# Kernel optimization log

Measured on AMD Instinct MI355X. Metric: run time of the kernel, lower is better.

The kernel has to match this reference:

```python
import jax, jax.numpy as jnp
import numpy as np

B, T, C = 2, 2048, 2048
H, HKV, D = 16, 4, 128
THETA = 10000.0
G = H // HKV  # kv groups


def _rope_tables(seq_len, dim, theta):
    inv_freq = 1.0 / theta ** (jnp.arange(0, dim, 2, dtype=jnp.float32) / dim)
    t = jnp.arange(seq_len, dtype=jnp.float32)
    freqs = jnp.outer(t, inv_freq)                 # [T, D/2]
    emb = jnp.concatenate([freqs, freqs], axis=-1)  # [T, D]
    return jnp.cos(emb)[None, None], jnp.sin(emb)[None, None]  # [1,1,T,D]


def _rotate_half(x):
    x1, x2 = jnp.split(x, 2, axis=-1)
    return jnp.concatenate([-x2, x1], axis=-1)


def setup_inputs() -> dict:
    key = jax.random.key(0)
    ks = jax.random.split(key, 6)
    x = jax.random.normal(ks[0], (B, T, C), dtype=jnp.float32)
    s = 0.02
    Wq = jax.random.normal(ks[1], (C, H * D), dtype=jnp.float32) * s
    Wk = jax.random.normal(ks[2], (C, HKV * D), dtype=jnp.float32) * s
    Wv = jax.random.normal(ks[3], (C, HKV * D), dtype=jnp.float32) * s
    Wo = jax.random.normal(ks[4], (H * D, C), dtype=jnp.float32) * s
    mask = jnp.tril(jnp.ones((T, T), dtype=jnp.int32))[None, None]  # causal [1,1,T,T]
    return {"x": x, "Wq": Wq, "Wk": Wk, "Wv": Wv, "Wo": Wo, "mask": mask}


def reference(x, Wq, Wk, Wv, Wo, mask):
    b, t, _ = x.shape
    q = (x @ Wq).reshape(b, t, H, D).transpose(0, 2, 1, 3)      # [B,H,T,D]
    k = (x @ Wk).reshape(b, t, HKV, D).transpose(0, 2, 1, 3)    # [B,HKV,T,D]
    v = (x @ Wv).reshape(b, t, HKV, D).transpose(0, 2, 1, 3)
    cos, sin = _rope_tables(t, D, THETA)
    q = q * cos + _rotate_half(q) * sin
    k = k * cos + _rotate_half(k) * sin
    # expand kv heads (repeat_interleave over head axis)
    k = jnp.repeat(k, G, axis=1)                                # [B,H,T,D]
    v = jnp.repeat(v, G, axis=1)
    attn = jnp.einsum('bhqd,bhkd->bhqk', q, k) / jnp.sqrt(jnp.float32(D))
    attn = jnp.where(mask == 0, jnp.float32(-jnp.inf), attn)
    attn = jax.nn.softmax(attn, axis=-1)
    out = jnp.einsum('bhqk,bhkd->bhqd', attn, v)                # [B,H,T,D]
    out = out.transpose(0, 2, 1, 3).reshape(b, t, H * D)
    return out @ Wo
```

## Files before the change

### kernel.cpp

```cpp
#include <hip/hip_runtime.h>
#include <math.h>

#define B_ 2
#define T_ 2048
#define C_ 2048
#define H_ 16
#define HKV_ 4
#define D_ 128
#define G_ (H_ / HKV_)
#define GK 2048

typedef float f32x4 __attribute__((ext_vector_type(4)));
typedef __bf16 bf16x8 __attribute__((ext_vector_type(8)));

static __device__ __forceinline__ f32x4 mfma16(bf16x8 a, bf16x8 b, f32x4 c) {
    return __builtin_amdgcn_mfma_f32_16x16x32_bf16(a, b, c, 0, 0, 0);
}

__global__ __launch_bounds__(256)
void conv_f32_bf16(const float* __restrict__ src, __bf16* __restrict__ dst, int n8)
{
    const int i = blockIdx.x * blockDim.x + threadIdx.x;
    if (i >= n8) return;
    const float4 a = *(const float4*)&src[(size_t)i * 8];
    const float4 b = *(const float4*)&src[(size_t)i * 8 + 4];
    bf16x8 o;
    o[0] = (__bf16)a.x; o[1] = (__bf16)a.y; o[2] = (__bf16)a.z; o[3] = (__bf16)a.w;
    o[4] = (__bf16)b.x; o[5] = (__bf16)b.y; o[6] = (__bf16)b.z; o[7] = (__bf16)b.w;
    *(bf16x8*)&dst[(size_t)i * 8] = o;
}

__global__ __launch_bounds__(256)
void tconv(const float* __restrict__ src, __bf16* __restrict__ dst, int N)
{
    __shared__ __bf16 tl[32][34];
    const int tx = threadIdx.x;
    const int ty = threadIdx.y;
    const int k0 = blockIdx.x * 32;
    const int n0 = blockIdx.y * 32;

    #pragma unroll
    for (int i = 0; i < 4; ++i) {
        const int r = ty + i * 8;
        tl[r][tx] = (__bf16)src[(size_t)(k0 + r) * N + n0 + tx];
    }
    __syncthreads();
    #pragma unroll
    for (int i = 0; i < 4; ++i) {
        const int r = ty + i * 8;
        dst[(size_t)(n0 + r) * GK + k0 + tx] = tl[tx][r];
    }
}

#define LSTR 72

#define GEMM_MAIN(At, Bt)                                                       \
    __shared__ __bf16 As[128 * LSTR];                                           \
    __shared__ __bf16 Bs[128 * LSTR];                                           \
    const int tid = threadIdx.x;                                                \
    const int wave = tid >> 6, lane = tid & 63;                                 \
    const int a = lane & 15, bq = lane >> 4;                                    \
    const int wr = wave >> 1, wc = wave & 1;                                    \
    f32x4 acc[4][4];                                                            \
    _Pragma("unroll")                                                           \
    for (int mi = 0; mi < 4; ++mi)                                              \
        _Pragma("unroll")                                                       \
        for (int ni = 0; ni < 4; ++ni) acc[mi][ni] = (f32x4){0.f,0.f,0.f,0.f};  \
    for (int k0 = 0; k0 < GK; k0 += 64) {                                       \
        __syncthreads();                                                        \
        _Pragma("unroll")                                                       \
        for (int i = 0; i < 4; ++i) {                                           \
            const int idx = i * 256 + tid;                                      \
            const int r = idx >> 3, c8 = (idx & 7) * 8;                         \
            *(bf16x8*)&As[r * LSTR + c8] =                                      \
                *(const bf16x8*)&(At)[(size_t)r * GK + k0 + c8];                \
            *(bf16x8*)&Bs[r * LSTR + c8] =                                      \
                *(const bf16x8*)&(Bt)[(size_t)r * GK + k0 + c8];                \
        }                                                                       \
        __syncthreads();                                                        \
        _Pragma("unroll")                                                       \
        for (int ks = 0; ks < 2; ++ks) {                                        \
            bf16x8 af[4], bfr[4];                                               \
            _Pragma("unroll")                                                   \
            for (int mi = 0; mi < 4; ++mi)                                      \
                af[mi] = *(const bf16x8*)&As[(wr*64 + mi*16 + a) * LSTR + ks*32 + bq*8]; \
            _Pragma("unroll")                                                   \
            for (int ni = 0; ni < 4; ++ni)                                      \
                bfr[ni] = *(const bf16x8*)&Bs[(wc*64 + ni*16 + a) * LSTR + ks*32 + bq*8]; \
            _Pragma("unroll")                                                   \
            for (int mi = 0; mi < 4; ++mi)                                      \
                _Pragma("unroll")                                               \
                for (int ni = 0; ni < 4; ++ni)                                  \
                    acc[mi][ni] = mfma16(af[mi], bfr[ni], acc[mi][ni]);         \
        }                                                                       \
    }

__global__ __launch_bounds__(256)
void gemm_qkv_mfma(const __bf16* __restrict__ xb,
                   const __bf16* __restrict__ wqt,
                   const __bf16* __restrict__ wkt,
                   const __bf16* __restrict__ wvt,
                   __bf16* __restrict__ qbuf,
                   __bf16* __restrict__ kbuf,
                   __bf16* __restrict__ vbuf)
{
    const int n0 = blockIdx.x * 128;
    const int m0 = blockIdx.y * 128;
    const __bf16* Btp; __bf16* outb; int NH, nloc;
    if (n0 < 2048)      { Btp = wqt + (size_t)n0 * GK;          outb = qbuf; NH = 16; nloc = n0; }
    else if (n0 < 2560) { Btp = wkt + (size_t)(n0 - 2048) * GK; outb = kbuf; NH = 4;  nloc = n0 - 2048; }
    else                { Btp = wvt + (size_t)(n0 - 2560) * GK; outb = vbuf; NH = 4;  nloc = n0 - 2560; }
    const __bf16* Atp = xb + (size_t)m0 * GK;

    GEMM_MAIN(Atp, Btp)

    const int b  = m0 >> 11;
    const int t0 = m0 & (T_ - 1);
    const int h0 = nloc >> 7;
    __bf16* op = outb + (size_t)(b * NH + h0) * T_ * D_;
    #pragma unroll
    for (int mi = 0; mi < 4; ++mi)
        #pragma unroll
        for (int ni = 0; ni < 4; ++ni)
            #pragma unroll
            for (int rr = 0; rr < 4; ++rr) {
                const int row = t0 + wr * 64 + mi * 16 + bq * 4 + rr;
                const int col = wc * 64 + ni * 16 + a;
                op[(size_t)row * D_ + col] = (__bf16)acc[mi][ni][rr];
            }
}

__global__ __launch_bounds__(256)
void gemm_out_mfma(const __bf16* __restrict__ ab,
                   const __bf16* __restrict__ wot,
                   float* __restrict__ outp)
{
    const int n0 = blockIdx.x * 128;
    const int m0 = blockIdx.y * 128;
    const __bf16* Atp = ab + (size_t)m0 * GK;
    const __bf16* Btp = wot + (size_t)n0 * GK;

    GEMM_MAIN(Atp, Btp)

    #pragma unroll
    for (int mi = 0; mi < 4; ++mi)
        #pragma unroll
        for (int ni = 0; ni < 4; ++ni)
            #pragma unroll
            for (int rr = 0; rr < 4; ++rr) {
                const int row = m0 + wr * 64 + mi * 16 + bq * 4 + rr;
                const int col = n0 + wc * 64 + ni * 16 + a;
                outp[(size_t)row * C_ + col] = acc[mi][ni][rr];
            }
}

__global__ void rope_bf16(__bf16* __restrict__ buf)
{
    const int idx = blockIdx.x * blockDim.x + threadIdx.x;
    const int jj  = idx & 31;
    const int row = idx >> 5;
    const int t   = row & (T_ - 1);
    const int d   = jj * 2;

    const float LOG_THETA = 9.210340371976184f;
    const float f1 = (float)t * __expf(-(float)d       * (LOG_THETA / 64.0f));
    const float f2 = (float)t * __expf(-(float)(d + 1) * (LOG_THETA / 64.0f));
    float s1, c1, s2, c2;
    __sincosf(f1, &s1, &c1);
    __sincosf(f2, &s2, &c2);

    __bf16* p = buf + (size_t)row * D_ + d;
    const float x1a = (float)p[0],  x1b = (float)p[1];
    const float x2a = (float)p[64], x2b = (float)p[65];
    p[0]  = (__bf16)(x1a * c1 - x2a * s1);
    p[1]  = (__bf16)(x1b * c2 - x2b * s2);
    p[64] = (__bf16)(x2a * c1 + x1a * s1);
    p[65] = (__bf16)(x2b * c2 + x1b * s2);
}

__global__ __launch_bounds__(256)
void transpose_v(const __bf16* __restrict__ vb, __bf16* __restrict__ vtb)
{
    __shared__ __bf16 tl[32][33];
    const int tx = threadIdx.x;
    const int ty = threadIdx.y;
    const int t0 = blockIdx.x * 32;
    const int d0 = blockIdx.y * 32;
    const int bh = blockIdx.z;

    const __bf16* src = vb + ((size_t)bh * T_ + t0) * D_ + d0;
    #pragma unroll
    for (int i = 0; i < 4; ++i) {
        const int r = ty + i * 8;
        tl[r][tx] = src[(size_t)r * D_ + tx];
    }
    __syncthreads();
    __bf16* dst = vtb + ((size_t)bh * D_ + d0) * T_ + t0;
    #pragma unroll
    for (int i = 0; i < 4; ++i) {
        const int dl = ty + i * 8;
        dst[(size_t)dl * T_ + tx] = tl[tx][dl];
    }
}

#define KS_STRIDE 136
#define PS_STRIDE 76

__global__ __launch_bounds__(512)
void flash_attn_mfma(const __bf16* __restrict__ qb,
                     const __bf16* __restrict__ kb,
                     const __bf16* __restrict__ vtb,
                     __bf16* __restrict__ abuf)
{
    __shared__ __bf16 KsL[64 * KS_STRIDE];
    __shared__ __bf16 VsL[2 * 128 * 4 * 8];
    __shared__ __bf16 PsL[8 * 16 * PS_STRIDE];

    const int tid  = threadIdx.x;
    const int wave = tid >> 6;
    const int lane = tid & 63;
    const int a    = lane & 15;
    const int bq   = lane >> 4;

    const int pair = blockIdx.x;
    const int bh   = blockIdx.y;
    const int b    = bh >> 4;
    const int h    = bh & 15;
    const int kvh  = h >> 2;

    const __bf16* kg  = kb  + (size_t)(b * HKV_ + kvh) * T_ * D_;
    const __bf16* vtg = vtb + (size_t)(b * HKV_ + kvh) * D_ * T_;

    const float scale = 0.08838834764831845f;

    for (int half = 0; half < 2; ++half) {
        const int qti = half == 0 ? (15 - pair) : pair;
        const int qt0 = qti * 128;
        const int ntiles = 2 * qti + 2;

        const __bf16* qg = qb + ((size_t)(b * H_ + h) * T_ + qt0 + wave * 16) * D_;
        bf16x8 qf[4];
        #pragma unroll
        for (int ks = 0; ks < 4; ++ks)
            qf[ks] = *(const bf16x8*)&qg[(size_t)a * D_ + ks * 32 + bq * 8];

        f32x4 oacc[8];
        #pragma unroll
        for (int dt = 0; dt < 8; ++dt) oacc[dt] = (f32x4){0.f, 0.f, 0.f, 0.f};
        float m_r[4] = {-INFINITY, -INFINITY, -INFINITY, -INFINITY};
        float l_r[4] = {0.f, 0.f, 0.f, 0.f};

        bf16x8 kpre[2], vpre[2];
        #pragma unroll
        for (int it = 0; it < 2; ++it) {
            const int idx = it * 512 + tid;
            const int r = idx >> 4, c8 = (idx & 15) * 8;
            kpre[it] = *(const bf16x8*)&kg[(size_t)r * D_ + c8];
            const int bo = idx & 3, dd = (idx >> 2) & 127, ss2 = idx >> 9;
            vpre[it] = *(const bf16x8*)&vtg[(size_t)dd * T_ + ss2 * 32 + bo * 8];
        }
        __syncthreads();
        #pragma unroll
        for (int it = 0; it < 2; ++it) {
            const int idx = it * 512 + tid;
            const int r = idx >> 4, c8 = (idx & 15) * 8;
            *(bf16x8*)&KsL[r * KS_STRIDE + c8] = kpre[it];
            *(bf16x8*)&VsL[idx * 8] = vpre[it];
        }
        __syncthreads();

        for (int kt = 0; kt < ntiles; ++kt) {
            const int k0 = kt * 64;
            if (kt + 1 < ntiles) {
                const int k0n = k0 + 64;
                #pragma unroll
                for (int it = 0; it < 2; ++it) {
                    const int idx = it * 512 + tid;
                    const int r = idx >> 4, c8 = (idx & 15) * 8;
                    kpre[it] = *(const bf16x8*)&kg[(size_t)(k0n + r) * D_ + c8];
                    const int bo = idx & 3, dd = (idx >> 2) & 127, ss2 = idx >> 9;
                    vpre[it] = *(const bf16x8*)&vtg[(size_t)dd * T_ + k0n + ss2 * 32 + bo * 8];
                }
            }

            f32x4 sacc[4];
            #pragma unroll
            for (int nt = 0; nt < 4; ++nt) {
                sacc[nt] = (f32x4){0.f, 0.f, 0.f, 0.f};
                #pragma unroll
                for (int ks = 0; ks < 4; ++ks) {
                    bf16x8 kf = *(const bf16x8*)&KsL[(nt * 16 + a) * KS_STRIDE + ks * 32 + bq * 8];
                    sacc[nt] = mfma16(qf[ks], kf, sacc[nt]);
                }
            }

            float p[4][4];
            float mrow[4] = {-INFINITY, -INFINITY, -INFINITY, -INFINITY};
            #pragma unroll
            for (int nt = 0; nt < 4; ++nt) {
                const int kc = k0 + nt * 16 + a;
                #pragma unroll
                for (int r = 0; r < 4; ++r) {
                    const int qrow = qt0 + wave * 16 + bq * 4 + r;
                    float s = sacc[nt][r] * scale;
                    s = (kc <= qrow) ? s : -INFINITY;
                    p[nt][r] = s;
                    mrow[r] = fmaxf(mrow[r], s);
                }
            }
            #pragma unroll
            for (int off = 1; off < 16; off <<= 1)
                #pragma unroll
                for (int r = 0; r < 4; ++r)
                    mrow[r] = fmaxf(mrow[r], __shfl_xor(mrow[r], off));

            float corr[4], psum[4];
            #pragma unroll
            for (int r = 0; r < 4; ++r) {
                const float mnew = fmaxf(m_r[r], mrow[r]);
                corr[r] = __expf(m_r[r] - mnew);
                m_r[r] = mnew;
                psum[r] = 0.f;
                #pragma unroll
                for (int nt = 0; nt < 4; ++nt) {
                    const float pe = __expf(p[nt][r] - mnew);
                    p[nt][r] = pe;
                    psum[r] += pe;
                }
            }
            #pragma unroll
            for (int off = 1; off < 16; off <<= 1)
                #pragma unroll
                for (int r = 0; r < 4; ++r)
                    psum[r] += __shfl_xor(psum[r], off);
            #pragma unroll
            for (int r = 0; r < 4; ++r) l_r[r] = l_r[r] * corr[r] + psum[r];

            #pragma unroll
            for (int dt = 0; dt < 8; ++dt)
                #pragma unroll
                for (int r = 0; r < 4; ++r) oacc[dt][r] *= corr[r];

            #pragma unroll
            for (int nt = 0; nt < 4; ++nt)
                #pragma unroll
                for (int r = 0; r < 4; ++r)
                    PsL[(wave * 16 + bq * 4 + r) * PS_STRIDE + nt * 16 + a] = (__bf16)p[nt][r];

            bf16x8 pf[2];
            #pragma unroll
            for (int ss = 0; ss < 2; ++ss)
                pf[ss] = *(const bf16x8*)&PsL[(wave * 16 + a) * PS_STRIDE + ss * 32 + bq * 8];
            #pragma unroll
            for (int dt = 0; dt < 8; ++dt) {
                #pragma unroll
                for (int ss = 0; ss < 2; ++ss) {
                    bf16x8 vf = *(const bf16x8*)&VsL[ss * 4096 + (dt * 16 + a) * 32 + bq * 8];
                    oacc[dt] = mfma16(pf[ss], vf, oacc[dt]);
                }
            }

            __syncthreads();
            if (kt + 1 < ntiles) {
                #pragma unroll
                for (int it = 0; it < 2; ++it) {
                    const int idx = it * 512 + tid;
                    const int r = idx >> 4, c8 = (idx & 15) * 8;
                    *(bf16x8*)&KsL[r * KS_STRIDE + c8] = kpre[it];
                    *(bf16x8*)&VsL[idx * 8] = vpre[it];
                }
                __syncthreads();
            }
        }

        float invl[4];
        #pragma unroll
        for (int r = 0; r < 4; ++r) invl[r] = 1.f / l_r[r];
        #pragma unroll
        for (int dt = 0; dt < 8; ++dt)
            #pragma unroll
            for (int r = 0; r < 4; ++r) {
                const int qrow = qt0 + wave * 16 + bq * 4 + r;
                abuf[((size_t)(b * T_) + qrow) * (H_ * D_) + h * D_ + dt * 16 + a] =
                    (__bf16)(oacc[dt][r] * invl[r]);
            }
    }
}

extern "C" void kernel_launch(void* const* d_in, const int* in_sizes, int n_in,
                              void* d_out, int out_size, void* d_ws, size_t ws_size,
                              hipStream_t stream)
{
    (void)in_sizes; (void)n_in; (void)out_size; (void)ws_size;
    const float* x  = (const float*)d_in[0];
    const float* Wq = (const float*)d_in[1];
    const float* Wk = (const float*)d_in[2];
    const float* Wv = (const float*)d_in[3];
    const float* Wo = (const float*)d_in[4];
    float* out = (float*)d_out;

    __bf16* xb  = (__bf16*)d_ws;
    __bf16* wqt = xb  + (size_t)4096 * 2048;
    __bf16* wkt = wqt + (size_t)2048 * 2048;
    __bf16* wvt = wkt + (size_t)512 * 2048;
    __bf16* wot = wvt + (size_t)512 * 2048;
    __bf16* qb  = wot + (size_t)2048 * 2048;
    __bf16* kb  = qb  + (size_t)B_ * H_   * T_ * D_;
    __bf16* vb  = kb  + (size_t)B_ * HKV_ * T_ * D_;
    __bf16* vtb = vb  + (size_t)B_ * HKV_ * T_ * D_;
    __bf16* ab  = vtb + (size_t)B_ * HKV_ * T_ * D_;

    hipLaunchKernelGGL(conv_f32_bf16, dim3(4096), dim3(256), 0, stream,
                       x, xb, (int)((size_t)B_ * T_ * C_ / 8));
    hipLaunchKernelGGL(tconv, dim3(64, 64), dim3(32, 8), 0, stream, Wq, wqt, 2048);
    hipLaunchKernelGGL(tconv, dim3(64, 16), dim3(32, 8), 0, stream, Wk, wkt, 512);
    hipLaunchKernelGGL(tconv, dim3(64, 16), dim3(32, 8), 0, stream, Wv, wvt, 512);
    hipLaunchKernelGGL(tconv, dim3(64, 64), dim3(32, 8), 0, stream, Wo, wot, 2048);

    hipLaunchKernelGGL(gemm_qkv_mfma, dim3(24, 32), dim3(256), 0, stream,
                       xb, wqt, wkt, wvt, qb, kb, vb);

    hipLaunchKernelGGL(rope_bf16, dim3(B_ * H_ * T_ * 32 / 256), dim3(256), 0, stream, qb);
    hipLaunchKernelGGL(rope_bf16, dim3(B_ * HKV_ * T_ * 32 / 256), dim3(256), 0, stream, kb);

    hipLaunchKernelGGL(transpose_v, dim3(T_ / 32, D_ / 32, B_ * HKV_), dim3(32, 8), 0, stream,
                       vb, vtb);

    hipLaunchKernelGGL(flash_attn_mfma, dim3(8, B_ * H_), dim3(512), 0, stream,
                       qb, kb, vtb, ab);

    hipLaunchKernelGGL(gemm_out_mfma, dim3(16, 32), dim3(256), 0, stream,
                       ab, wot, out);
}
```

Baseline: 374.3 us.

## Use direct global-to-LDS loads in GEMM and skip masked attention tiles

The GEMM tile loads now use the global_load_lds builtin, writing straight into unpadded LDS tiles instead of staging through registers. The flash-attention kernel skips fully masked key tiles per wave, applies the causal mask only on diagonal tiles, and uses exp2 with a log2e-folded scale. It also pads the V LDS layout with a stride to reduce bank conflicts. Risks include LDS bank conflicts from the unpadded GEMM tiles, whether the direct-load lane-to-LDS layout matches the builtin's semantics, and divergence between waves around the shared barriers.

```diff
diff --git a/kernel.cpp b/kernel.cpp
--- a/kernel.cpp
+++ b/kernel.cpp
@@ -17,6 +17,13 @@
     return __builtin_amdgcn_mfma_f32_16x16x32_bf16(a, b, c, 0, 0, 0);
 }
 
+static __device__ __forceinline__ void gload16(const __bf16* g, __bf16* l) {
+    __builtin_amdgcn_global_load_lds(
+        (const __attribute__((address_space(1))) unsigned int*)g,
+        (__attribute__((address_space(3))) unsigned int*)l,
+        16, 0, 0);
+}
+
 __global__ __launch_bounds__(256)
 void conv_f32_bf16(const float* __restrict__ src, __bf16* __restrict__ dst, int n8)
 {
@@ -52,41 +59,39 @@
     }
 }
 
-#define LSTR 72
-
 #define GEMM_MAIN(At, Bt)                                                       \
-    __shared__ __bf16 As[128 * LSTR];                                           \
-    __shared__ __bf16 Bs[128 * LSTR];                                           \
+    __shared__ __bf16 As[128 * 64];                                             \
+    __shared__ __bf16 Bs[128 * 64];                                             \
     const int tid = threadIdx.x;                                                \
     const int wave = tid >> 6, lane = tid & 63;                                 \
     const int a = lane & 15, bq = lane >> 4;                                    \
     const int wr = wave >> 1, wc = wave & 1;                                    \
+    const int srow = wave * 32 + (lane >> 3);                        \
+    const int scol = (lane & 7) * 8;                                            \
     f32x4 acc[4][4];                                                            \
     _Pragma("unroll")                                                           \
     for (int mi = 0; mi < 4; ++mi)                                              \
         _Pragma("unroll")                                                       \
         for (int ni = 0; ni < 4; ++ni) acc[mi][ni] = (f32x4){0.f,0.f,0.f,0.f};  \
     for (int k0 = 0; k0 < GK; k0 += 64) {                                       \
-        __syncthreads();                                                        \
+        __syncthreads();                       \
         _Pragma("unroll")                                                       \
         for (int i = 0; i < 4; ++i) {                                           \
-            const int idx = i * 256 + tid;                                      \
-            const int r = idx >> 3, c8 = (idx & 7) * 8;                         \
-            *(bf16x8*)&As[r * LSTR + c8] =                                      \
-                *(const bf16x8*)&(At)[(size_t)r * GK + k0 + c8];                \
-            *(bf16x8*)&Bs[r * LSTR + c8] =                                      \
-                *(const bf16x8*)&(Bt)[(size_t)r * GK + k0 + c8];                \
+            gload16(&(At)[(size_t)(srow + i * 8) * GK + k0 + scol],             \
+                    &As[(wave * 32 + i * 8) * 64]);                             \
+            gload16(&(Bt)[(size_t)(srow + i * 8) * GK + k0 + scol],             \
+                    &Bs[(wave * 32 + i * 8) * 64]);                             \
         }                                                                       \
-        __syncthreads();                                                        \
+        __syncthreads();                \
         _Pragma("unroll")                                                       \
         for (int ks = 0; ks < 2; ++ks) {                                        \
             bf16x8 af[4], bfr[4];                                               \
             _Pragma("unroll")                                                   \
             for (int mi = 0; mi < 4; ++mi)                                      \
-                af[mi] = *(const bf16x8*)&As[(wr*64 + mi*16 + a) * LSTR + ks*32 + bq*8]; \
+                af[mi] = *(const bf16x8*)&As[(wr*64 + mi*16 + a) * 64 + ks*32 + bq*8]; \
             _Pragma("unroll")                                                   \
             for (int ni = 0; ni < 4; ++ni)                                      \
-                bfr[ni] = *(const bf16x8*)&Bs[(wc*64 + ni*16 + a) * LSTR + ks*32 + bq*8]; \
+                bfr[ni] = *(const bf16x8*)&Bs[(wc*64 + ni*16 + a) * 64 + ks*32 + bq*8]; \
             _Pragma("unroll")                                                   \
             for (int mi = 0; mi < 4; ++mi)                                      \
                 _Pragma("unroll")                                               \
@@ -204,6 +209,7 @@
 }
 
 #define KS_STRIDE 136
+#define VS_STRIDE 36
 #define PS_STRIDE 76
 
 __global__ __launch_bounds__(512)
@@ -213,7 +219,7 @@
                      __bf16* __restrict__ abuf)
 {
     __shared__ __bf16 KsL[64 * KS_STRIDE];
-    __shared__ __bf16 VsL[2 * 128 * 4 * 8];
+    __shared__ __bf16 VsL[2 * 128 * VS_STRIDE];
     __shared__ __bf16 PsL[8 * 16 * PS_STRIDE];
 
     const int tid  = threadIdx.x;
@@ -231,14 +237,15 @@
     const __bf16* kg  = kb  + (size_t)(b * HKV_ + kvh) * T_ * D_;
     const __bf16* vtg = vtb + (size_t)(b * HKV_ + kvh) * D_ * T_;
 
-    const float scale = 0.08838834764831845f;
+    const float scale2 = 0.12750176129424902f;
 
     for (int half = 0; half < 2; ++half) {
         const int qti = half == 0 ? (15 - pair) : pair;
         const int qt0 = qti * 128;
         const int ntiles = 2 * qti + 2;
-
-        const __bf16* qg = qb + ((size_t)(b * H_ + h) * T_ + qt0 + wave * 16) * D_;
+        const int qrow_lo = qt0 + wave * 16;
+
+        const __bf16* qg = qb + ((size_t)(b * H_ + h) * T_ + qrow_lo) * D_;
         bf16x8 qf[4];
         #pragma unroll
         for (int ks = 0; ks < 4; ++ks)
@@ -265,7 +272,8 @@
             const int idx = it * 512 + tid;
             const int r = idx >> 4, c8 = (idx & 15) * 8;
             *(bf16x8*)&KsL[r * KS_STRIDE + c8] = kpre[it];
-            *(bf16x8*)&VsL[idx * 8] = vpre[it];
+            const int bo = idx & 3, dd = (idx >> 2) & 127, ss2 = idx >> 9;
+            *(bf16x8*)&VsL[(ss2 * 128 + dd) * VS_STRIDE + bo * 8] = vpre[it];
         }
         __syncthreads();
 
@@ -283,80 +291,85 @@
                 }
             }
 
-            f32x4 sacc[4];
-            #pragma unroll
-            for (int nt = 0; nt < 4; ++nt) {
-                sacc[nt] = (f32x4){0.f, 0.f, 0.f, 0.f};
-                #pragma unroll
-                for (int ks = 0; ks < 4; ++ks) {
-                    bf16x8 kf = *(const bf16x8*)&KsL[(nt * 16 + a) * KS_STRIDE + ks * 32 + bq * 8];
-                    sacc[nt] = mfma16(qf[ks], kf, sacc[nt]);
-                }
-            }
-
-            float p[4][4];
-            float mrow[4] = {-INFINITY, -INFINITY, -INFINITY, -INFINITY};
-            #pragma unroll
-            for (int nt = 0; nt < 4; ++nt) {
-                const int kc = k0 + nt * 16 + a;
+            if (k0 <= qrow_lo + 15) {
+                f32x4 sacc[4];
+                #pragma unroll
+                for (int nt = 0; nt < 4; ++nt) {
+                    sacc[nt] = (f32x4){0.f, 0.f, 0.f, 0.f};
+                    #pragma unroll
+                    for (int ks = 0; ks < 4; ++ks) {
+                        bf16x8 kf = *(const bf16x8*)&KsL[(nt * 16 + a) * KS_STRIDE + ks * 32 + bq * 8];
+                        sacc[nt] = mfma16(qf[ks], kf, sacc[nt]);
+                    }
+                }
+
+                float p[4][4];
+                float mrow[4] = {-INFINITY, -INFINITY, -INFINITY, -INFINITY};
+                const bool needmask = (k0 + 63 > qrow_lo);
+                #pragma unroll
+                for (int nt = 0; nt < 4; ++nt) {
+                    const int kc = k0 + nt * 16 + a;
+                    #pragma unroll
+                    for (int r = 0; r < 4; ++r) {
+                        float s = sacc[nt][r] * scale2;
+                        if (needmask) {
+                            const int qrow = qrow_lo + bq * 4 + r;
+                            s = (kc <= qrow) ? s : -INFINITY;
+                        }
+                        p[nt][r] = s;
+                        mrow[r] = fmaxf(mrow[r], s);
+                    }
+                }
+                #pragma unroll
+                for (int off = 1; off < 16; off <<= 1)
+                    #pragma unroll
+                    for (int r = 0; r < 4; ++r)
+                        mrow[r] = fmaxf(mrow[r], __shfl_xor(mrow[r], off));
+
+                float corr[4], psum[4];
                 #pragma unroll
                 for (int r = 0; r < 4; ++r) {
-                    const int qrow = qt0 + wave * 16 + bq * 4 + r;
-                    float s = sacc[nt][r] * scale;
-                    s = (kc <= qrow) ? s : -INFINITY;
-                    p[nt][r] = s;
-                    mrow[r] = fmaxf(mrow[r], s);
-                }
-            }
-            #pragma unroll
-            for (int off = 1; off < 16; off <<= 1)
-                #pragma unroll
-                for (int r = 0; r < 4; ++r)
-                    mrow[r] = fmaxf(mrow[r], __shfl_xor(mrow[r], off));
-
-            float corr[4], psum[4];
-            #pragma unroll
-            for (int r = 0; r < 4; ++r) {
-                const float mnew = fmaxf(m_r[r], mrow[r]);
-                corr[r] = __expf(m_r[r] - mnew);
-                m_r[r] = mnew;
-                psum[r] = 0.f;
-                #pragma unroll
-                for (int nt = 0; nt < 4; ++nt) {
-                    const float pe = __expf(p[nt][r] - mnew);
-                    p[nt][r] = pe;
-                    psum[r] += pe;
-                }
-            }
-            #pragma unroll
-            for (int off = 1; off < 16; off <<= 1)
-                #pragma unroll
-                for (int r = 0; r < 4; ++r)
-                    psum[r] += __shfl_xor(psum[r], off);
-            #pragma unroll
-            for (int r = 0; r < 4; ++r) l_r[r] = l_r[r] * corr[r] + psum[r];
-
-            #pragma unroll
-            for (int dt = 0; dt < 8; ++dt)
-                #pragma unroll
-                for (int r = 0; r < 4; ++r) oacc[dt][r] *= corr[r];
-
-            #pragma unroll
-            for (int nt = 0; nt < 4; ++nt)
-                #pragma unroll
-                for (int r = 0; r < 4; ++r)
-                    PsL[(wave * 16 + bq * 4 + r) * PS_STRIDE + nt * 16 + a] = (__bf16)p[nt][r];
-
-            bf16x8 pf[2];
-            #pragma unroll
-            for (int ss = 0; ss < 2; ++ss)
-                pf[ss] = *(const bf16x8*)&PsL[(wave * 16 + a) * PS_STRIDE + ss * 32 + bq * 8];
-            #pragma unroll
-            for (int dt = 0; dt < 8; ++dt) {
-                #pragma unroll
-                for (int ss = 0; ss < 2; ++ss) {
-                    bf16x8 vf = *(const bf16x8*)&VsL[ss * 4096 + (dt * 16 + a) * 32 + bq * 8];
-                    oacc[dt] = mfma16(pf[ss], vf, oacc[dt]);
+                    const float mnew = fmaxf(m_r[r], mrow[r]);
+                    corr[r] = exp2f(m_r[r] - mnew);
+                    m_r[r] = mnew;
+                    psum[r] = 0.f;
+                    #pragma unroll
+                    for (int nt = 0; nt < 4; ++nt) {
+                        const float pe = exp2f(p[nt][r] - mnew);
+                        p[nt][r] = pe;
+                        psum[r] += pe;
+                    }
+                }
+                #pragma unroll
+                for (int off = 1; off < 16; off <<= 1)
+                    #pragma unroll
+                    for (int r = 0; r < 4; ++r)
+                        psum[r] += __shfl_xor(psum[r], off);
+                #pragma unroll
+                for (int r = 0; r < 4; ++r) l_r[r] = l_r[r] * corr[r] + psum[r];
+
+                #pragma unroll
+                for (int dt = 0; dt < 8; ++dt)
+                    #pragma unroll
+                    for (int r = 0; r < 4; ++r) oacc[dt][r] *= corr[r];
+
+                #pragma unroll
+                for (int nt = 0; nt < 4; ++nt)
+                    #pragma unroll
+                    for (int r = 0; r < 4; ++r)
+                        PsL[(wave * 16 + bq * 4 + r) * PS_STRIDE + nt * 16 + a] = (__bf16)p[nt][r];
+
+                bf16x8 pf[2];
+                #pragma unroll
+                for (int ss = 0; ss < 2; ++ss)
+                    pf[ss] = *(const bf16x8*)&PsL[(wave * 16 + a) * PS_STRIDE + ss * 32 + bq * 8];
+                #pragma unroll
+                for (int dt = 0; dt < 8; ++dt) {
+                    #pragma unroll
+                    for (int ss = 0; ss < 2; ++ss) {
+                        bf16x8 vf = *(const bf16x8*)&VsL[(ss * 128 + dt * 16 + a) * VS_STRIDE + bq * 8];
+                        oacc[dt] = mfma16(pf[ss], vf, oacc[dt]);
+                    }
                 }
             }
 
@@ -367,7 +380,8 @@
                     const int idx = it * 512 + tid;
                     const int r = idx >> 4, c8 = (idx & 15) * 8;
                     *(bf16x8*)&KsL[r * KS_STRIDE + c8] = kpre[it];
-                    *(bf16x8*)&VsL[idx * 8] = vpre[it];
+                    const int bo = idx & 3, dd = (idx >> 2) & 127, ss2 = idx >> 9;
+                    *(bf16x8*)&VsL[(ss2 * 128 + dd) * VS_STRIDE + bo * 8] = vpre[it];
                 }
                 __syncthreads();
             }
@@ -380,7 +394,7 @@
         for (int dt = 0; dt < 8; ++dt)
             #pragma unroll
             for (int r = 0; r < 4; ++r) {
-                const int qrow = qt0 + wave * 16 + bq * 4 + r;
+                const int qrow = qrow_lo + bq * 4 + r;
                 abuf[((size_t)(b * T_) + qrow) * (H_ * D_) + h * D_ + dt * 16 + a] =
                     (__bf16)(oacc[dt][r] * invl[r]);
             }
```

Result: slower. 386.9 us (+3.4%).
